# Optimization experiments

Hardware: AMD Instinct MI355X
Metric: run time of the kernel (lower is better)

## Reference

```python
import jax, jax.numpy as jnp
import numpy as np

B, T = 64, 1024
EMB = 10          # embedding_dim
H = 64            # hidden_size
NH = 2            # attention heads
IN = 3 * EMB      # 30 = GRU input_size
GAMMA = 1.0


def rbf(d):
    # BondExpansionRBF: exp(-gamma * |center - d|^2), centers = 1..10
    centers = jnp.arange(1, EMB + 1, dtype=d.dtype)          # [10]
    return jnp.exp(-GAMMA * (centers - d[..., None]) ** 2)   # [..., 10]


def gru_layer(x, w_ih, w_hh, b_ih, b_hh):
    # x: [B,T,D] -> [B,T,H]; torch GRU gate order: r, z, n
    Bn = x.shape[0]
    Hn = w_hh.shape[1]
    xw = jnp.einsum('btd,gd->btg', x, w_ih) + b_ih           # [B,T,3H] precomputed input proj

    def step(h, xt):
        gh = h @ w_hh.T + b_hh
        xr, xz, xn = jnp.split(xt, 3, axis=-1)
        hr, hz, hn = jnp.split(gh, 3, axis=-1)
        r = jax.nn.sigmoid(xr + hr)
        z = jax.nn.sigmoid(xz + hz)
        n = jnp.tanh(xn + r * hn)
        h = (1.0 - z) * n + z * h
        return h, h

    _, ys = jax.lax.scan(step, jnp.zeros((Bn, Hn), x.dtype), jnp.swapaxes(xw, 0, 1))
    return jnp.swapaxes(ys, 0, 1)


def mha(x, in_w, in_b, out_w, out_b):
    # torch nn.MultiheadAttention (batch_first, self-attn), eval mode
    Bn, Tn, E = x.shape
    Hd = E // NH
    qkv = x @ in_w.T + in_b                                   # [B,T,3E]
    q, k, v = jnp.split(qkv, 3, axis=-1)

    def heads(t):
        return t.reshape(Bn, Tn, NH, Hd).transpose(0, 2, 1, 3)  # [B,NH,T,Hd]

    q, k, v = heads(q), heads(k), heads(v)
    scores = jnp.einsum('bhqd,bhkd->bhqk', q, k) / jnp.asarray(np.sqrt(Hd), x.dtype)
    a = jax.nn.softmax(scores, axis=-1)
    o = jnp.einsum('bhqk,bhkd->bhqd', a, v).transpose(0, 2, 1, 3).reshape(Bn, Tn, E)
    return o @ out_w.T + out_b


def forward(atom_idx, bond_dist, emb, w_ih0, w_hh0, b_ih0, b_hh0,
            w_ih1, w_hh1, b_ih1, b_hh1, in_w1, in_b1, out_w1, out_b1,
            in_w2, in_b2, out_w2, out_b2, w_l, b_l, w_l1, b_l1):
    idx_i = atom_idx[..., 0]
    idx_j = atom_idx[..., 1]
    # index 0 -> zero vector (padding semantics of the python-loop conditionals)
    e_i = jnp.where((idx_i != 0)[..., None], emb[idx_i], 0.0)   # [B,T,10]
    e_j = jnp.where((idx_j != 0)[..., None], emb[idx_j], 0.0)   # [B,T,10]
    d = jnp.where((idx_i != 0)[..., None], rbf(bond_dist), 0.0)  # [B,T,10]
    x = jnp.concatenate([e_i, e_j, d], axis=-1)                  # [B,T,30]

    g = gru_layer(x, w_ih0, w_hh0, b_ih0, b_hh0)
    g = gru_layer(g, w_ih1, w_hh1, b_ih1, b_hh1)
    a = mha(g, in_w1, in_b1, out_w1, out_b1)
    a = mha(a, in_w2, in_b2, out_w2, out_b2)

    last = a[:, -1, :]                                           # [B,H]
    h = jax.nn.relu(last @ w_l.T + b_l)                          # [B,32]
    out = h @ w_l1.T + b_l1                                      # [B,1]
    return out[:, 0]                                             # [B]


def setup_inputs() -> dict:
    key = jax.random.key(0)
    ks = jax.random.split(key, 20)

    def n(k, shape, s=0.05):
        return jax.random.normal(k, shape, jnp.float32) * s

    return {
        'atom_idx': jax.random.randint(ks[0], (B, T, 2), 0, 119),
        'bond_dist': jax.random.uniform(ks[1], (B, T), jnp.float32) * 10.0,
        'emb': n(ks[2], (119, EMB), 1.0),
        'w_ih0': n(ks[3], (3 * H, IN)), 'w_hh0': n(ks[4], (3 * H, H)),
        'b_ih0': n(ks[5], (3 * H,)), 'b_hh0': n(ks[6], (3 * H,)),
        'w_ih1': n(ks[7], (3 * H, H)), 'w_hh1': n(ks[8], (3 * H, H)),
        'b_ih1': n(ks[9], (3 * H,)), 'b_hh1': n(ks[10], (3 * H,)),
        'in_w1': n(ks[11], (3 * H, H)), 'in_b1': n(ks[12], (3 * H,)),
        'out_w1': n(ks[13], (H, H)), 'out_b1': jnp.zeros((H,), jnp.float32),
        'in_w2': n(ks[14], (3 * H, H)), 'in_b2': n(ks[15], (3 * H,)),
        'out_w2': n(ks[16], (H, H)), 'out_b2': jnp.zeros((H,), jnp.float32),
        'w_l': n(ks[17], (32, H)), 'b_l': jnp.zeros((32,), jnp.float32),
        'w_l1': n(ks[18], (1, 32)), 'b_l1': jnp.zeros((1,), jnp.float32),
    }


def reference(atom_idx, bond_dist, emb, w_ih0, w_hh0, b_ih0, b_hh0,
              w_ih1, w_hh1, b_ih1, b_hh1, in_w1, in_b1, out_w1, out_b1,
              in_w2, in_b2, out_w2, out_b2, w_l, b_l, w_l1, b_l1):
    return forward(atom_idx, bond_dist, emb, w_ih0, w_hh0, b_ih0, b_hh0,
                   w_ih1, w_hh1, b_ih1, b_hh1, in_w1, in_b1, out_w1, out_b1,
                   in_w2, in_b2, out_w2, out_b2, w_l, b_l, w_l1, b_l1)
```

## Files before the change

kernel.cpp:

```cpp
#include <hip/hip_runtime.h>

typedef unsigned int uint_t;
typedef float v2f __attribute__((ext_vector_type(2)));

#define BB 64
#define TT 1024

__device__ __forceinline__ float sigm(float x) { return 1.f / (1.f + __expf(-x)); }
__device__ __forceinline__ float tanh_f(float x) { float e = __expf(2.f * x); return 1.f - 2.f / (e + 1.f); }
__device__ __forceinline__ int finitef(float x) { return (x == x) && (fabsf(x) < 1e30f); }

__device__ __forceinline__ void spinwait(volatile int* f, int v) {
  if (*f >= v) { asm volatile("" ::: "memory"); return; }
  int it = 0;
  while (*f < v && it < (1 << 15)) { __builtin_amdgcn_s_sleep(1); ++it; }
  asm volatile("" ::: "memory");
}

__device__ __forceinline__ float feat(int b, int t, int j,
                                      const int* atom_idx, const float* bond_dist,
                                      const float* emb) {
  int ii = atom_idx[(b * TT + t) * 2 + 0];
  if (j < 10) {
    return ii ? emb[ii * 10 + j] : 0.f;
  } else if (j < 20) {
    int jj = atom_idx[(b * TT + t) * 2 + 1];
    return jj ? emb[jj * 10 + (j - 10)] : 0.f;
  } else {
    float d = bond_dist[b * TT + t];
    float c = (float)(j - 19);
    float df = c - d;
    return ii ? __expf(-df * df) : 0.f;
  }
}

extern "C" __global__ void __launch_bounds__(256)
k_xw0(const int* atom_idx, const float* bond_dist, const float* emb,
      const float* w_ih0, const float* b_ih0, float* xw0) {
  int b  = blockIdx.x >> 4;
  int t0 = (blockIdx.x & 15) << 6;
  int tid = threadIdx.x;
  __shared__ float xt[64 * 31];
  for (int i = tid; i < 64 * 30; i += 256) {
    int r = i / 30, j = i % 30;
    xt[r * 31 + j] = feat(b, t0 + r, j, atom_idx, bond_dist, emb);
  }
  __syncthreads();
  for (int L = tid; L < 64 * 192; L += 256) {
    int g = L >> 6, r = L & 63;
    const float* wr = w_ih0 + g * 30;
    const float* ar = &xt[r * 31];
    float acc = b_ih0[g];
    #pragma unroll
    for (int c = 0; c < 30; ++c) acc += wr[c] * ar[c];
    xw0[((size_t)b * TT + t0 + r) * 192 + g] = acc;
  }
}

__device__ __forceinline__ void gemm64(const float* __restrict__ act_g,
                                       const float* __restrict__ w,
                                       const float* __restrict__ bias,
                                       float* al,
                                       int G, int tid,
                                       float* out, int out_rstride, size_t out_base) {
  for (int i = tid; i < 64 * 64; i += 256) {
    int r = i >> 6, c = i & 63;
    al[r * 65 + c] = act_g[r * 64 + c];
  }
  __syncthreads();
  for (int L = tid; L < 64 * G; L += 256) {
    int g = L >> 6, r = L & 63;
    const float* wr = w + (size_t)g * 64;
    const float* ar = &al[r * 65];
    float acc = bias[g];
    #pragma unroll
    for (int c = 0; c < 64; ++c) acc += wr[c] * ar[c];
    out[out_base + (size_t)r * out_rstride + g] = acc;
  }
}

__device__ __forceinline__ void loadw2(const float* p, v2f* w2) {
  const float4* p4 = (const float4*)p;
  #pragma unroll
  for (int i = 0; i < 16; ++i) {
    float4 a = p4[i];
    v2f lo; lo.x = a.x; lo.y = a.y;
    v2f hi; hi.x = a.z; hi.y = a.w;
    w2[2 * i] = lo; w2[2 * i + 1] = hi;
  }
}

extern "C" __global__ void __launch_bounds__(192, 1)
k_grufused(const float* xw0, const float* w_hh0, const float* b_hh0,
           const float* w_ih1, const float* b_ih1,
           const float* w_hh1, const float* b_hh1, float* g1out) {
  int b    = blockIdx.x;
  int lane = threadIdx.x & 63;
  int wid  = threadIdx.x >> 6;
  __shared__ __align__(16) float h0ring[16][64];
  __shared__ __align__(16) float xwring[16][192];
  __shared__ __align__(16) float h1pp[2][64];
  __shared__ int flags[3];

  if (threadIdx.x < 3) flags[threadIdx.x] = -1;
  if (wid == 0) h0ring[15][lane] = 0.f;
  if (wid == 2) h1pp[0][lane] = 0.f;
  __syncthreads();

  volatile int* w0d = &flags[0];
  volatile int* w1d = &flags[1];
  volatile int* w2d = &flags[2];

  if (wid == 0) {
    v2f wr2[32], wz2[32], wn2[32];
    loadw2(w_hh0 + (size_t)lane * 64,        wr2);
    loadw2(w_hh0 + (size_t)(64 + lane) * 64, wz2);
    loadw2(w_hh0 + (size_t)(128 + lane) * 64, wn2);
    float br = b_hh0[lane], bz = b_hh0[64 + lane], bn = b_hh0[128 + lane];
    float hv = 0.f;
    const float* xwb = xw0 + (size_t)b * TT * 192;
    float xr0 = xwb[      lane], xz0 = xwb[ 64 + lane], xn0 = xwb[128 + lane];
    float xr1 = xwb[192 + lane], xz1 = xwb[256 + lane], xn1 = xwb[320 + lane];
    float xr2 = xwb[384 + lane], xz2 = xwb[448 + lane], xn2 = xwb[512 + lane];
    float xr3 = xwb[576 + lane], xz3 = xwb[640 + lane], xn3 = xwb[704 + lane];

    auto gstep = [&](int s, float xr, float xz, float xn) {
      const float4* hp4 = (const float4*)h0ring[(s + 15) & 15];
      v2f ar; ar.x = br; ar.y = 0.f;
      v2f az; az.x = bz; az.y = 0.f;
      v2f an; an.x = bn; an.y = 0.f;
      #pragma unroll
      for (int i = 0; i < 16; ++i) {
        float4 h4 = hp4[i];
        v2f hlo; hlo.x = h4.x; hlo.y = h4.y;
        v2f hhi; hhi.x = h4.z; hhi.y = h4.w;
        ar += wr2[2*i] * hlo; ar += wr2[2*i+1] * hhi;
        az += wz2[2*i] * hlo; az += wz2[2*i+1] * hhi;
        an += wn2[2*i] * hlo; an += wn2[2*i+1] * hhi;
      }
      float r = sigm(xr + (ar.x + ar.y));
      float z = sigm(xz + (az.x + az.y));
      float n = tanh_f(xn + r * (an.x + an.y));
      hv = (1.f - z) * n + z * hv;
      h0ring[s & 15][lane] = hv;
    };
    auto pf = [&](int s, float& a, float& bb_, float& c) {
      const float* xp = xwb + (size_t)s * 192;
      a = xp[lane]; bb_ = xp[64 + lane]; c = xp[128 + lane];
    };

    for (int s0 = 0; s0 < TT; s0 += 4) {
      if (s0 >= 16) spinwait(w1d, s0 - 13);
      bool dopf = (s0 < TT - 4);
      gstep(s0 + 0, xr0, xz0, xn0); if (dopf) pf(s0 + 4, xr0, xz0, xn0);
      gstep(s0 + 1, xr1, xz1, xn1); if (dopf) pf(s0 + 5, xr1, xz1, xn1);
      gstep(s0 + 2, xr2, xz2, xn2); if (dopf) pf(s0 + 6, xr2, xz2, xn2);
      gstep(s0 + 3, xr3, xz3, xn3); if (dopf) pf(s0 + 7, xr3, xz3, xn3);
      asm volatile("" ::: "memory");
      if (lane == 0) *w0d = s0 + 3;
    }
  } else if (wid == 1) {
    v2f wr2[32], wz2[32], wn2[32];
    loadw2(w_ih1 + (size_t)lane * 64,        wr2);
    loadw2(w_ih1 + (size_t)(64 + lane) * 64, wz2);
    loadw2(w_ih1 + (size_t)(128 + lane) * 64, wn2);
    float br = b_ih1[lane], bz = b_ih1[64 + lane], bn = b_ih1[128 + lane];

    for (int t0 = 0; t0 < TT; t0 += 4) {
      spinwait(w0d, t0 + 3);
      if (t0 >= 16) spinwait(w2d, t0 - 13);
      #pragma unroll
      for (int k = 0; k < 4; ++k) {
        int t = t0 + k;
        const float4* hp4 = (const float4*)h0ring[t & 15];
        v2f ar; ar.x = br; ar.y = 0.f;
        v2f az; az.x = bz; az.y = 0.f;
        v2f an; an.x = bn; an.y = 0.f;
        #pragma unroll
        for (int i = 0; i < 16; ++i) {
          float4 h4 = hp4[i];
          v2f hlo; hlo.x = h4.x; hlo.y = h4.y;
          v2f hhi; hhi.x = h4.z; hhi.y = h4.w;
          ar += wr2[2*i] * hlo; ar += wr2[2*i+1] * hhi;
          az += wz2[2*i] * hlo; az += wz2[2*i+1] * hhi;
          an += wn2[2*i] * hlo; an += wn2[2*i+1] * hhi;
        }
        xwring[t & 15][lane]       = ar.x + ar.y;
        xwring[t & 15][64 + lane]  = az.x + az.y;
        xwring[t & 15][128 + lane] = an.x + an.y;
      }
      asm volatile("" ::: "memory");
      if (lane == 0) *w1d = t0 + 3;
    }
  } else {
    v2f wr2[32], wz2[32], wn2[32];
    loadw2(w_hh1 + (size_t)lane * 64,        wr2);
    loadw2(w_hh1 + (size_t)(64 + lane) * 64, wz2);
    loadw2(w_hh1 + (size_t)(128 + lane) * 64, wn2);
    float br = b_hh1[lane], bz = b_hh1[64 + lane], bn = b_hh1[128 + lane];
    float hv = 0.f;
    float* houtb = g1out + (size_t)b * TT * 64 + lane;

    for (int t0 = 0; t0 < TT; t0 += 4) {
      spinwait(w1d, t0 + 3);
      #pragma unroll
      for (int k = 0; k < 4; ++k) {
        int t = t0 + k;
        float xr = xwring[t & 15][lane];
        float xz = xwring[t & 15][64 + lane];
        float xn = xwring[t & 15][128 + lane];
        const float4* hp4 = (const float4*)h1pp[t & 1];
        v2f ar; ar.x = br; ar.y = 0.f;
        v2f az; az.x = bz; az.y = 0.f;
        v2f an; an.x = bn; an.y = 0.f;
        #pragma unroll
        for (int i = 0; i < 16; ++i) {
          float4 h4 = hp4[i];
          v2f hlo; hlo.x = h4.x; hlo.y = h4.y;
          v2f hhi; hhi.x = h4.z; hhi.y = h4.w;
          ar += wr2[2*i] * hlo; ar += wr2[2*i+1] * hhi;
          az += wz2[2*i] * hlo; az += wz2[2*i+1] * hhi;
          an += wn2[2*i] * hlo; an += wn2[2*i+1] * hhi;
        }
        float r = sigm(xr + (ar.x + ar.y));
        float z = sigm(xz + (az.x + az.y));
        float n = tanh_f(xn + r * (an.x + an.y));
        hv = (1.f - z) * n + z * hv;
        h1pp[(t + 1) & 1][lane] = hv;
        houtb[(size_t)t * 64] = hv;
      }
      asm volatile("" ::: "memory");
      if (lane == 0) *w2d = t0 + 3;
    }
  }
}

extern "C" __global__ void __launch_bounds__(256)
k_qkv(const float* g1, const float* in_w1, const float* in_b1,
      float* q1, float* k1, float* v1) {
  int b  = blockIdx.x >> 4;
  int t0 = (blockIdx.x & 15) << 6;
  int tid = threadIdx.x;
  __shared__ float al[64 * 65];
  const float* act = g1 + ((size_t)b * TT + t0) * 64;
  for (int i = tid; i < 64 * 64; i += 256) {
    int r = i >> 6, c = i & 63;
    al[r * 65 + c] = act[r * 64 + c];
  }
  __syncthreads();
  for (int L = tid; L < 64 * 192; L += 256) {
    int g = L >> 6, r = L & 63;
    const float* wr = in_w1 + (size_t)g * 64;
    const float* ar = &al[r * 65];
    float acc = in_b1[g];
    #pragma unroll
    for (int c = 0; c < 64; ++c) acc += wr[c] * ar[c];
    int p = g / 64;
    int rem = g - p * 64;
    int hd = rem >> 5, d = rem & 31;
    float* outp = (p == 0) ? q1 : ((p == 1) ? k1 : v1);
    outp[(((size_t)b * 2 + hd) * TT + t0 + r) * 32 + d] = acc;
  }
}

extern "C" __global__ void __launch_bounds__(256, 2)
k_attn(const float* q1, const float* k1, const float* v1, float* po, float* ml) {
  int gid = blockIdx.x;
  int b   = gid >> 3;
  int h   = (gid >> 2) & 1;
  int seg = (gid >> 1) & 1;
  int qb  = gid & 1;
  int tid = threadIdx.x;
  int tq0 = qb * 512 + tid;
  __shared__ __align__(16) float Kt[64 * 32];
  __shared__ __align__(16) float Vt[64 * 32];
  float qa[32], qc[32], oa[32], oc[32];
  const float* qp0 = q1 + (((size_t)b * 2 + h) * TT + tq0) * 32;
  const float* qp1 = qp0 + 256 * 32;
  #pragma unroll
  for (int i = 0; i < 8; ++i) {
    float4 v0 = ((const float4*)qp0)[i];
    float4 v1r = ((const float4*)qp1)[i];
    qa[4*i] = v0.x; qa[4*i+1] = v0.y; qa[4*i+2] = v0.z; qa[4*i+3] = v0.w;
    qc[4*i] = v1r.x; qc[4*i+1] = v1r.y; qc[4*i+2] = v1r.z; qc[4*i+3] = v1r.w;
  }
  #pragma unroll
  for (int i = 0; i < 32; ++i) { oa[i] = 0.f; oc[i] = 0.f; }
  float m0 = -1e30f, l0 = 0.f, m1 = -1e30f, l1 = 0.f;
  const float scale = 0.17677669529663687f;
  const float4* kb = (const float4*)(k1 + ((size_t)b * 2 + h) * TT * 32);
  const float4* vb = (const float4*)(v1 + ((size_t)b * 2 + h) * TT * 32);
  int k0 = seg << 9;
  for (int kt = k0; kt < k0 + 512; kt += 64) {
    __syncthreads();
    ((float4*)Kt)[tid]       = kb[kt * 8 + tid];
    ((float4*)Kt)[tid + 256] = kb[kt * 8 + tid + 256];
    ((float4*)Vt)[tid]       = vb[kt * 8 + tid];
    ((float4*)Vt)[tid + 256] = vb[kt * 8 + tid + 256];
    __syncthreads();
    #pragma unroll 1
    for (int c0 = 0; c0 < 64; c0 += 8) {
      float sv0[8], sv1[8];
      #pragma unroll
      for (int j = 0; j < 8; ++j) {
        const float4* kr = (const float4*)&Kt[(c0 + j) * 32];
        float a0 = 0, a1 = 0, c0a = 0, c1a = 0;
        #pragma unroll
        for (int i = 0; i < 8; ++i) {
          float4 kv = kr[i];
          a0 += qa[4*i]   * kv.x; a1 += qa[4*i+1] * kv.y;
          a0 += qa[4*i+2] * kv.z; a1 += qa[4*i+3] * kv.w;
          c0a += qc[4*i]   * kv.x; c1a += qc[4*i+1] * kv.y;
          c0a += qc[4*i+2] * kv.z; c1a += qc[4*i+3] * kv.w;
        }
        sv0[j] = (a0 + a1) * scale;
        sv1[j] = (c0a + c1a) * scale;
      }
      float cm0 = sv0[0], cm1 = sv1[0];
      #pragma unroll
      for (int j = 1; j < 8; ++j) { cm0 = fmaxf(cm0, sv0[j]); cm1 = fmaxf(cm1, sv1[j]); }
      float mn0 = fmaxf(m0, cm0), mn1 = fmaxf(m1, cm1);
      float al0 = __expf(m0 - mn0), al1 = __expf(m1 - mn1);
      float ps0 = 0.f, ps1 = 0.f;
      #pragma unroll
      for (int j = 0; j < 8; ++j) {
        sv0[j] = __expf(sv0[j] - mn0); ps0 += sv0[j];
        sv1[j] = __expf(sv1[j] - mn1); ps1 += sv1[j];
      }
      l0 = l0 * al0 + ps0; m0 = mn0;
      l1 = l1 * al1 + ps1; m1 = mn1;
      #pragma unroll
      for (int i = 0; i < 8; ++i) {
        float4 A, C;
        A.x = oa[4*i] * al0; A.y = oa[4*i+1] * al0; A.z = oa[4*i+2] * al0; A.w = oa[4*i+3] * al0;
        C.x = oc[4*i] * al1; C.y = oc[4*i+1] * al1; C.z = oc[4*i+2] * al1; C.w = oc[4*i+3] * al1;
        #pragma unroll
        for (int j = 0; j < 8; ++j) {
          float4 vv = *(const float4*)&Vt[(c0 + j) * 32 + 4 * i];
          A.x += sv0[j] * vv.x; A.y += sv0[j] * vv.y; A.z += sv0[j] * vv.z; A.w += sv0[j] * vv.w;
          C.x += sv1[j] * vv.x; C.y += sv1[j] * vv.y; C.z += sv1[j] * vv.z; C.w += sv1[j] * vv.w;
        }
        oa[4*i] = A.x; oa[4*i+1] = A.y; oa[4*i+2] = A.z; oa[4*i+3] = A.w;
        oc[4*i] = C.x; oc[4*i+1] = C.y; oc[4*i+2] = C.z; oc[4*i+3] = C.w;
      }
    }
  }
  size_t rb0 = (((size_t)(b * 2 + h)) * 2 + seg) * TT + tq0;
  size_t rb1 = rb0 + 256;
  float* op0 = po + rb0 * 32;
  float* op1 = po + rb1 * 32;
  #pragma unroll
  for (int i = 0; i < 8; ++i) {
    float4 s0; s0.x = oa[4*i]; s0.y = oa[4*i+1]; s0.z = oa[4*i+2]; s0.w = oa[4*i+3];
    float4 s1; s1.x = oc[4*i]; s1.y = oc[4*i+1]; s1.z = oc[4*i+2]; s1.w = oc[4*i+3];
    ((float4*)op0)[i] = s0;
    ((float4*)op1)[i] = s1;
  }
  ml[rb0 * 2 + 0] = m0; ml[rb0 * 2 + 1] = l0;
  ml[rb1 * 2 + 0] = m1; ml[rb1 * 2 + 1] = l1;
}

extern "C" __global__ void __launch_bounds__(256)
k_attn_comb(const float* po, const float* ml, float* attnO) {
  int row = blockIdx.x * 256 + threadIdx.x;
  int bh = row >> 10;
  int t  = row & 1023;
  int b = bh >> 1, h = bh & 1;
  size_t r0 = ((size_t)bh * 2 + 0) * TT + t;
  size_t r1 = ((size_t)bh * 2 + 1) * TT + t;
  float m0 = ml[r0 * 2], l0 = ml[r0 * 2 + 1];
  float m1 = ml[r1 * 2], l1 = ml[r1 * 2 + 1];
  float m = fmaxf(m0, m1);
  float w0 = __expf(m0 - m), w1 = __expf(m1 - m);
  float inv = 1.f / (w0 * l0 + w1 * l1);
  w0 *= inv; w1 *= inv;
  const float4* p0 = (const float4*)(po + r0 * 32);
  const float4* p1 = (const float4*)(po + r1 * 32);
  float* op = attnO + ((size_t)b * TT + t) * 64 + h * 32;
  #pragma unroll
  for (int i = 0; i < 8; ++i) {
    float4 a = p0[i], c = p1[i], r;
    r.x = a.x * w0 + c.x * w1; r.y = a.y * w0 + c.y * w1;
    r.z = a.z * w0 + c.z * w1; r.w = a.w * w0 + c.w * w1;
    ((float4*)op)[i] = r;
  }
}

extern "C" __global__ void __launch_bounds__(256)
k_oproj(const float* attnO, const float* out_w1, const float* out_b1, float* a1) {
  int b  = blockIdx.x >> 4;
  int t0 = (blockIdx.x & 15) << 6;
  __shared__ float al[64 * 65];
  gemm64(attnO + ((size_t)b * TT + t0) * 64, out_w1, out_b1, al, 64, threadIdx.x,
         a1, 64, ((size_t)b * TT + t0) * 64);
}

extern "C" __global__ void __launch_bounds__(256)
k_mha2kv(const float* a1, const float* in_w2, const float* in_b2,
         float* s2, float* v2) {
  int b  = blockIdx.x >> 4;
  int t0 = (blockIdx.x & 15) << 6;
  int tid = threadIdx.x;
  __shared__ float a1r[64 * 65];
  __shared__ float q2s[64];
  __shared__ float alast[64];
  if (tid < 64) alast[tid] = a1[((size_t)b * TT + (TT - 1)) * 64 + tid];
  for (int i = tid; i < 4096; i += 256) {
    int r = i >> 6, e = i & 63;
    a1r[r * 65 + e] = a1[((size_t)b * TT + t0 + r) * 64 + e];
  }
  __syncthreads();
  if (tid < 64) {
    float acc = in_b2[tid];
    const float* wr = in_w2 + (size_t)tid * 64;
    #pragma unroll
    for (int e = 0; e < 64; ++e) acc += alast[e] * wr[e];
    q2s[tid] = acc;
  }
  __syncthreads();
  int tt = tid & 63;
  int role = tid >> 6;
  const float* ar = &a1r[tt * 65];
  const float scale = 0.17677669529663687f;
  if (role < 2) {
    float s = 0.f;
    for (int d = 0; d < 32; ++d) {
      int row = 64 + role * 32 + d;
      const float* wr = in_w2 + (size_t)row * 64;
      float acc = in_b2[row];
      #pragma unroll
      for (int e = 0; e < 64; ++e) acc += ar[e] * wr[e];
      s += q2s[row - 64] * acc;
    }
    s2[((size_t)b * 2 + role) * TT + t0 + tt] = s * scale;
  } else {
    int half = role - 2;
    for (int d = 0; d < 32; ++d) {
      int vd = half * 32 + d;
      int row = 128 + vd;
      const float* wr = in_w2 + (size_t)row * 64;
      float acc = in_b2[row];
      #pragma unroll
      for (int e = 0; e < 64; ++e) acc += ar[e] * wr[e];
      v2[((size_t)b * TT + t0 + tt) * 64 + vd] = acc;
    }
  }
}

extern "C" __global__ void __launch_bounds__(256)
k_final(const float* s2, const float* v2,
        const float* out_w2, const float* out_b2,
        const float* w_l, const float* b_l,
        const float* w_l1, const float* b_l1,
        float* out) {
  int b = blockIdx.x;
  int tid = threadIdx.x;
  __shared__ float sm[2 * 1024];
  __shared__ float red[8];
  __shared__ float invl[2];
  __shared__ float opart[4 * 64];
  __shared__ float of[64];
  __shared__ float a2[64];
  __shared__ float hbuf[32];
  __shared__ int bad;
  if (tid == 0) bad = 0;
  for (int i = tid; i < 2048; i += 256) sm[i] = s2[(size_t)b * 2 * TT + i];
  __syncthreads();
  int lane = tid & 63;
  int wid = tid >> 6;
  for (int hh = 0; hh < 2; ++hh) {
    float mx = -1e30f;
    for (int i = tid; i < 1024; i += 256) mx = fmaxf(mx, sm[hh * 1024 + i]);
    #pragma unroll
    for (int off = 32; off > 0; off >>= 1) mx = fmaxf(mx, __shfl_down(mx, off));
    if (lane == 0) red[wid] = mx;
    __syncthreads();
    if (tid == 0) red[4] = fmaxf(fmaxf(red[0], red[1]), fmaxf(red[2], red[3]));
    __syncthreads();
    mx = red[4];
    float s = 0.f;
    for (int i = tid; i < 1024; i += 256) {
      float e = __expf(sm[hh * 1024 + i] - mx);
      sm[hh * 1024 + i] = e;
      s += e;
    }
    #pragma unroll
    for (int off = 32; off > 0; off >>= 1) s += __shfl_down(s, off);
    if (lane == 0) red[wid] = s;
    __syncthreads();
    if (tid == 0) invl[hh] = 1.f / (red[0] + red[1] + red[2] + red[3]);
    __syncthreads();
  }
  {
    int dp = tid & 63;
    int part = tid >> 6;
    int hh = dp >> 5;
    float acc = 0.f;
    for (int t = part * 256; t < part * 256 + 256; ++t)
      acc += sm[hh * 1024 + t] * v2[((size_t)b * TT + t) * 64 + dp];
    opart[part * 64 + dp] = acc;
  }
  __syncthreads();
  if (tid < 64) {
    float o = (opart[tid] + opart[64 + tid] + opart[128 + tid] + opart[192 + tid]) * invl[tid >> 5];
    of[tid] = o;
    if (!finitef(o)) bad = 1;
  }
  __syncthreads();
  if (tid < 64) {
    float acc = out_b2[tid];
    const float* wr = out_w2 + (size_t)tid * 64;
    #pragma unroll
    for (int d = 0; d < 64; ++d) acc += of[d] * wr[d];
    a2[tid] = acc;
  }
  __syncthreads();
  if (tid < 32) {
    float acc = b_l[tid];
    const float* wr = w_l + (size_t)tid * 64;
    #pragma unroll
    for (int e = 0; e < 64; ++e) acc += a2[e] * wr[e];
    hbuf[tid] = fmaxf(acc, 0.f);
  }
  __syncthreads();
  if (tid == 0) {
    float acc = b_l1[0];
    #pragma unroll
    for (int j = 0; j < 32; ++j) acc += hbuf[j] * w_l1[j];
    out[b] = bad ? 777.0f : acc;
  }
}

extern "C" void kernel_launch(void* const* d_in, const int* in_sizes, int n_in,
                              void* d_out, int out_size, void* d_ws, size_t ws_size,
                              hipStream_t stream) {
  const int*   atom_idx  = (const int*)d_in[0];
  const float* bond_dist = (const float*)d_in[1];
  const float* emb       = (const float*)d_in[2];
  const float* w_ih0     = (const float*)d_in[3];
  const float* w_hh0     = (const float*)d_in[4];
  const float* b_ih0     = (const float*)d_in[5];
  const float* b_hh0     = (const float*)d_in[6];
  const float* w_ih1     = (const float*)d_in[7];
  const float* w_hh1     = (const float*)d_in[8];
  const float* b_ih1     = (const float*)d_in[9];
  const float* b_hh1     = (const float*)d_in[10];
  const float* in_w1     = (const float*)d_in[11];
  const float* in_b1     = (const float*)d_in[12];
  const float* out_w1    = (const float*)d_in[13];
  const float* out_b1    = (const float*)d_in[14];
  const float* in_w2     = (const float*)d_in[15];
  const float* in_b2     = (const float*)d_in[16];
  const float* out_w2    = (const float*)d_in[17];
  const float* out_b2    = (const float*)d_in[18];
  const float* w_l       = (const float*)d_in[19];
  const float* b_l       = (const float*)d_in[20];
  const float* w_l1      = (const float*)d_in[21];
  const float* b_l1      = (const float*)d_in[22];

  char* ws = (char*)d_ws;
  float* X  = (float*)(ws);
  float* A  = (float*)(ws + 50331648);
  float* Bq = (float*)(ws + 67108864);
  float* D  = (float*)(ws + 83886080);
  float* q1 = X;
  float* k1 = X + 4194304;
  float* v1 = X + 8388608;
  float* po = (float*)(ws + 16777216);
  float* ml = Bq;

  k_xw0      <<<dim3(1024), dim3(256), 0, stream>>>(atom_idx, bond_dist, emb, w_ih0, b_ih0, X);
  k_grufused <<<dim3(64),   dim3(192), 0, stream>>>(X, w_hh0, b_hh0, w_ih1, b_ih1, w_hh1, b_hh1, Bq);
  k_qkv      <<<dim3(1024), dim3(256), 0, stream>>>(Bq, in_w1, in_b1, q1, k1, v1);
  k_attn     <<<dim3(512),  dim3(256), 0, stream>>>(q1, k1, v1, po, ml);
  k_attn_comb<<<dim3(512),  dim3(256), 0, stream>>>(po, ml, A);
  k_oproj    <<<dim3(1024), dim3(256), 0, stream>>>(A, out_w1, out_b1, Bq);
  k_mha2kv   <<<dim3(1024), dim3(256), 0, stream>>>(Bq, in_w2, in_b2, D, X);
  k_final    <<<dim3(64),   dim3(256), 0, stream>>>(D, X, out_w2, out_b2, w_l, b_l, w_l1, b_l1, (float*)d_out);
}
```

Measured before the change: 1.297 ms.

## Merge GRU layer-1 input projection into layer-0 wave; register-block small GEMMs

The fused two-layer GRU kernel drops from three waves to two. The layer-0 wave now also computes the layer-1 input projection of the previous hidden state in the same pass over h, so the ring buffer for h0 shrinks to a ping-pong buffer and one inter-wave handoff disappears. Separately, the xw0, qkv and out-projection GEMMs are restructured so each thread computes 8 outputs per row, reusing each shared-memory activation load across them. The trade-off is that the layer-0 wave now carries twice the weight registers and roughly twice the FMA work per step on what is the serial critical path.

```diff
diff --git a/kernel.cpp b/kernel.cpp
--- a/kernel.cpp
+++ b/kernel.cpp
@@ -46,36 +46,50 @@
     xt[r * 31 + j] = feat(b, t0 + r, j, atom_idx, bond_dist, emb);
   }
   __syncthreads();
-  for (int L = tid; L < 64 * 192; L += 256) {
-    int g = L >> 6, r = L & 63;
-    const float* wr = w_ih0 + g * 30;
-    const float* ar = &xt[r * 31];
-    float acc = b_ih0[g];
-    #pragma unroll
-    for (int c = 0; c < 30; ++c) acc += wr[c] * ar[c];
-    xw0[((size_t)b * TT + t0 + r) * 192 + g] = acc;
-  }
-}
-
-__device__ __forceinline__ void gemm64(const float* __restrict__ act_g,
-                                       const float* __restrict__ w,
-                                       const float* __restrict__ bias,
-                                       float* al,
-                                       int G, int tid,
-                                       float* out, int out_rstride, size_t out_base) {
+  int r = tid & 63, gq = tid >> 6;
+  const float* ar = &xt[r * 31];
+  for (int g0 = gq * 8; g0 < 192; g0 += 32) {
+    float acc[8];
+    #pragma unroll
+    for (int j = 0; j < 8; ++j) acc[j] = b_ih0[g0 + j];
+    #pragma unroll
+    for (int c = 0; c < 30; ++c) {
+      float a = ar[c];
+      #pragma unroll
+      for (int j = 0; j < 8; ++j) acc[j] += a * w_ih0[(g0 + j) * 30 + c];
+    }
+    #pragma unroll
+    for (int j = 0; j < 8; ++j)
+      xw0[((size_t)b * TT + t0 + r) * 192 + g0 + j] = acc[j];
+  }
+}
+
+__device__ __forceinline__ void gemm64b(const float* __restrict__ act_g,
+                                        const float* __restrict__ w,
+                                        const float* __restrict__ bias,
+                                        float* al,
+                                        int G, int tid,
+                                        float* out, int out_rstride, size_t out_base) {
   for (int i = tid; i < 64 * 64; i += 256) {
     int r = i >> 6, c = i & 63;
     al[r * 65 + c] = act_g[r * 64 + c];
   }
   __syncthreads();
-  for (int L = tid; L < 64 * G; L += 256) {
-    int g = L >> 6, r = L & 63;
-    const float* wr = w + (size_t)g * 64;
-    const float* ar = &al[r * 65];
-    float acc = bias[g];
-    #pragma unroll
-    for (int c = 0; c < 64; ++c) acc += wr[c] * ar[c];
-    out[out_base + (size_t)r * out_rstride + g] = acc;
+  int r = tid & 63, gq = tid >> 6;
+  const float* ar = &al[r * 65];
+  for (int g0 = gq * 8; g0 < G; g0 += 32) {
+    float acc[8];
+    #pragma unroll
+    for (int j = 0; j < 8; ++j) acc[j] = bias[g0 + j];
+    #pragma unroll
+    for (int c = 0; c < 64; ++c) {
+      float a = ar[c];
+      #pragma unroll
+      for (int j = 0; j < 8; ++j) acc[j] += a * w[(size_t)(g0 + j) * 64 + c];
+    }
+    #pragma unroll
+    for (int j = 0; j < 8; ++j)
+      out[out_base + (size_t)r * out_rstride + g0 + j] = acc[j];
   }
 }
 
@@ -90,33 +104,37 @@
   }
 }
 
-extern "C" __global__ void __launch_bounds__(192, 1)
+extern "C" __global__ void __launch_bounds__(128, 1)
 k_grufused(const float* xw0, const float* w_hh0, const float* b_hh0,
            const float* w_ih1, const float* b_ih1,
            const float* w_hh1, const float* b_hh1, float* g1out) {
   int b    = blockIdx.x;
   int lane = threadIdx.x & 63;
   int wid  = threadIdx.x >> 6;
-  __shared__ __align__(16) float h0ring[16][64];
+  __shared__ __align__(16) float h0pp[2][64];
   __shared__ __align__(16) float xwring[16][192];
   __shared__ __align__(16) float h1pp[2][64];
-  __shared__ int flags[3];
-
-  if (threadIdx.x < 3) flags[threadIdx.x] = -1;
-  if (wid == 0) h0ring[15][lane] = 0.f;
-  if (wid == 2) h1pp[0][lane] = 0.f;
+  __shared__ int flags[2];
+
+  if (threadIdx.x < 2) flags[threadIdx.x] = -1;
+  if (wid == 0) h0pp[0][lane] = 0.f;
+  if (wid == 1) h1pp[0][lane] = 0.f;
   __syncthreads();
 
   volatile int* w0d = &flags[0];
   volatile int* w1d = &flags[1];
-  volatile int* w2d = &flags[2];
 
   if (wid == 0) {
     v2f wr2[32], wz2[32], wn2[32];
-    loadw2(w_hh0 + (size_t)lane * 64,        wr2);
-    loadw2(w_hh0 + (size_t)(64 + lane) * 64, wz2);
+    v2f ur2[32], uz2[32], un2[32];
+    loadw2(w_hh0 + (size_t)lane * 64,         wr2);
+    loadw2(w_hh0 + (size_t)(64 + lane) * 64,  wz2);
     loadw2(w_hh0 + (size_t)(128 + lane) * 64, wn2);
+    loadw2(w_ih1 + (size_t)lane * 64,         ur2);
+    loadw2(w_ih1 + (size_t)(64 + lane) * 64,  uz2);
+    loadw2(w_ih1 + (size_t)(128 + lane) * 64, un2);
     float br = b_hh0[lane], bz = b_hh0[64 + lane], bn = b_hh0[128 + lane];
+    float cr = b_ih1[lane], cz = b_ih1[64 + lane], cn = b_ih1[128 + lane];
     float hv = 0.f;
     const float* xwb = xw0 + (size_t)b * TT * 192;
     float xr0 = xwb[      lane], xz0 = xwb[ 64 + lane], xn0 = xwb[128 + lane];
@@ -125,24 +143,35 @@
     float xr3 = xwb[576 + lane], xz3 = xwb[640 + lane], xn3 = xwb[704 + lane];
 
     auto gstep = [&](int s, float xr, float xz, float xn) {
-      const float4* hp4 = (const float4*)h0ring[(s + 15) & 15];
-      v2f ar; ar.x = br; ar.y = 0.f;
-      v2f az; az.x = bz; az.y = 0.f;
-      v2f an; an.x = bn; an.y = 0.f;
+      const float4* hp4 = (const float4*)h0pp[s & 1];
+      v2f ar_; ar_.x = br; ar_.y = 0.f;
+      v2f az_; az_.x = bz; az_.y = 0.f;
+      v2f an_; an_.x = bn; an_.y = 0.f;
+      v2f ur_; ur_.x = cr; ur_.y = 0.f;
+      v2f uz_; uz_.x = cz; uz_.y = 0.f;
+      v2f un_; un_.x = cn; un_.y = 0.f;
       #pragma unroll
       for (int i = 0; i < 16; ++i) {
         float4 h4 = hp4[i];
         v2f hlo; hlo.x = h4.x; hlo.y = h4.y;
         v2f hhi; hhi.x = h4.z; hhi.y = h4.w;
-        ar += wr2[2*i] * hlo; ar += wr2[2*i+1] * hhi;
-        az += wz2[2*i] * hlo; az += wz2[2*i+1] * hhi;
-        an += wn2[2*i] * hlo; an += wn2[2*i+1] * hhi;
+        ar_ += wr2[2*i] * hlo; ar_ += wr2[2*i+1] * hhi;
+        az_ += wz2[2*i] * hlo; az_ += wz2[2*i+1] * hhi;
+        an_ += wn2[2*i] * hlo; an_ += wn2[2*i+1] * hhi;
+        ur_ += ur2[2*i] * hlo; ur_ += ur2[2*i+1] * hhi;
+        uz_ += uz2[2*i] * hlo; uz_ += uz2[2*i+1] * hhi;
+        un_ += un2[2*i] * hlo; un_ += un2[2*i+1] * hhi;
       }
-      float r = sigm(xr + (ar.x + ar.y));
-      float z = sigm(xz + (az.x + az.y));
-      float n = tanh_f(xn + r * (an.x + an.y));
+      float r = sigm(xr + (ar_.x + ar_.y));
+      float z = sigm(xz + (az_.x + az_.y));
+      float n = tanh_f(xn + r * (an_.x + an_.y));
       hv = (1.f - z) * n + z * hv;
-      h0ring[s & 15][lane] = hv;
+      h0pp[(s + 1) & 1][lane] = hv;
+      if (s > 0) {
+        xwring[(s - 1) & 15][lane]       = ur_.x + ur_.y;
+        xwring[(s - 1) & 15][64 + lane]  = uz_.x + uz_.y;
+        xwring[(s - 1) & 15][128 + lane] = un_.x + un_.y;
+      }
     };
     auto pf = [&](int s, float& a, float& bb_, float& c) {
       const float* xp = xwb + (size_t)s * 192;
@@ -150,59 +179,46 @@
     };
 
     for (int s0 = 0; s0 < TT; s0 += 4) {
-      if (s0 >= 16) spinwait(w1d, s0 - 13);
+      if (s0 >= 16) spinwait(w1d, s0 - 14);
       bool dopf = (s0 < TT - 4);
       gstep(s0 + 0, xr0, xz0, xn0); if (dopf) pf(s0 + 4, xr0, xz0, xn0);
       gstep(s0 + 1, xr1, xz1, xn1); if (dopf) pf(s0 + 5, xr1, xz1, xn1);
       gstep(s0 + 2, xr2, xz2, xn2); if (dopf) pf(s0 + 6, xr2, xz2, xn2);
       gstep(s0 + 3, xr3, xz3, xn3); if (dopf) pf(s0 + 7, xr3, xz3, xn3);
       asm volatile("" ::: "memory");
-      if (lane == 0) *w0d = s0 + 3;
-    }
-  } else if (wid == 1) {
-    v2f wr2[32], wz2[32], wn2[32];
-    loadw2(w_ih1 + (size_t)lane * 64,        wr2);
-    loadw2(w_ih1 + (size_t)(64 + lane) * 64, wz2);
-    loadw2(w_ih1 + (size_t)(128 + lane) * 64, wn2);
-    float br = b_ih1[lane], bz = b_ih1[64 + lane], bn = b_ih1[128 + lane];
-
-    for (int t0 = 0; t0 < TT; t0 += 4) {
-      spinwait(w0d, t0 + 3);
-      if (t0 >= 16) spinwait(w2d, t0 - 13);
-      #pragma unroll
-      for (int k = 0; k < 4; ++k) {
-        int t = t0 + k;
-        const float4* hp4 = (const float4*)h0ring[t & 15];
-        v2f ar; ar.x = br; ar.y = 0.f;
-        v2f az; az.x = bz; az.y = 0.f;
-        v2f an; an.x = bn; an.y = 0.f;
-        #pragma unroll
-        for (int i = 0; i < 16; ++i) {
-          float4 h4 = hp4[i];
-          v2f hlo; hlo.x = h4.x; hlo.y = h4.y;
-          v2f hhi; hhi.x = h4.z; hhi.y = h4.w;
-          ar += wr2[2*i] * hlo; ar += wr2[2*i+1] * hhi;
-          az += wz2[2*i] * hlo; az += wz2[2*i+1] * hhi;
-          an += wn2[2*i] * hlo; an += wn2[2*i+1] * hhi;
-        }
-        xwring[t & 15][lane]       = ar.x + ar.y;
-        xwring[t & 15][64 + lane]  = az.x + az.y;
-        xwring[t & 15][128 + lane] = an.x + an.y;
+      if (lane == 0) *w0d = s0 + 2;
+    }
+    {
+      const float4* hp4 = (const float4*)h0pp[TT & 1];
+      v2f ur_; ur_.x = cr; ur_.y = 0.f;
+      v2f uz_; uz_.x = cz; uz_.y = 0.f;
+      v2f un_; un_.x = cn; un_.y = 0.f;
+      #pragma unroll
+      for (int i = 0; i < 16; ++i) {
+        float4 h4 = hp4[i];
+        v2f hlo; hlo.x = h4.x; hlo.y = h4.y;
+        v2f hhi; hhi.x = h4.z; hhi.y = h4.w;
+        ur_ += ur2[2*i] * hlo; ur_ += ur2[2*i+1] * hhi;
+        uz_ += uz2[2*i] * hlo; uz_ += uz2[2*i+1] * hhi;
+        un_ += un2[2*i] * hlo; un_ += un2[2*i+1] * hhi;
       }
+      xwring[(TT - 1) & 15][lane]       = ur_.x + ur_.y;
+      xwring[(TT - 1) & 15][64 + lane]  = uz_.x + uz_.y;
+      xwring[(TT - 1) & 15][128 + lane] = un_.x + un_.y;
       asm volatile("" ::: "memory");
-      if (lane == 0) *w1d = t0 + 3;
+      if (lane == 0) *w0d = TT - 1;
     }
   } else {
     v2f wr2[32], wz2[32], wn2[32];
-    loadw2(w_hh1 + (size_t)lane * 64,        wr2);
-    loadw2(w_hh1 + (size_t)(64 + lane) * 64, wz2);
+    loadw2(w_hh1 + (size_t)lane * 64,         wr2);
+    loadw2(w_hh1 + (size_t)(64 + lane) * 64,  wz2);
     loadw2(w_hh1 + (size_t)(128 + lane) * 64, wn2);
     float br = b_hh1[lane], bz = b_hh1[64 + lane], bn = b_hh1[128 + lane];
     float hv = 0.f;
     float* houtb = g1out + (size_t)b * TT * 64 + lane;
 
     for (int t0 = 0; t0 < TT; t0 += 4) {
-      spinwait(w1d, t0 + 3);
+      spinwait(w0d, t0 + 3);
       #pragma unroll
       for (int k = 0; k < 4; ++k) {
         int t = t0 + k;
@@ -210,27 +226,27 @@
         float xz = xwring[t & 15][64 + lane];
         float xn = xwring[t & 15][128 + lane];
         const float4* hp4 = (const float4*)h1pp[t & 1];
-        v2f ar; ar.x = br; ar.y = 0.f;
-        v2f az; az.x = bz; az.y = 0.f;
-        v2f an; an.x = bn; an.y = 0.f;
+        v2f ar_; ar_.x = br; ar_.y = 0.f;
+        v2f az_; az_.x = bz; az_.y = 0.f;
+        v2f an_; an_.x = bn; an_.y = 0.f;
         #pragma unroll
         for (int i = 0; i < 16; ++i) {
           float4 h4 = hp4[i];
           v2f hlo; hlo.x = h4.x; hlo.y = h4.y;
           v2f hhi; hhi.x = h4.z; hhi.y = h4.w;
-          ar += wr2[2*i] * hlo; ar += wr2[2*i+1] * hhi;
-          az += wz2[2*i] * hlo; az += wz2[2*i+1] * hhi;
-          an += wn2[2*i] * hlo; an += wn2[2*i+1] * hhi;
+          ar_ += wr2[2*i] * hlo; ar_ += wr2[2*i+1] * hhi;
+          az_ += wz2[2*i] * hlo; az_ += wz2[2*i+1] * hhi;
+          an_ += wn2[2*i] * hlo; an_ += wn2[2*i+1] * hhi;
         }
-        float r = sigm(xr + (ar.x + ar.y));
-        float z = sigm(xz + (az.x + az.y));
-        float n = tanh_f(xn + r * (an.x + an.y));
+        float r = sigm(xr + (ar_.x + ar_.y));
+        float z = sigm(xz + (az_.x + az_.y));
+        float n = tanh_f(xn + r * (an_.x + an_.y));
         hv = (1.f - z) * n + z * hv;
         h1pp[(t + 1) & 1][lane] = hv;
         houtb[(size_t)t * 64] = hv;
       }
       asm volatile("" ::: "memory");
-      if (lane == 0) *w2d = t0 + 3;
+      if (lane == 0) *w1d = t0 + 3;
     }
   }
 }
@@ -248,18 +264,26 @@
     al[r * 65 + c] = act[r * 64 + c];
   }
   __syncthreads();
-  for (int L = tid; L < 64 * 192; L += 256) {
-    int g = L >> 6, r = L & 63;
-    const float* wr = in_w1 + (size_t)g * 64;
-    const float* ar = &al[r * 65];
-    float acc = in_b1[g];
-    #pragma unroll
-    for (int c = 0; c < 64; ++c) acc += wr[c] * ar[c];
-    int p = g / 64;
-    int rem = g - p * 64;
-    int hd = rem >> 5, d = rem & 31;
+  int r = tid & 63, gq = tid >> 6;
+  const float* ar = &al[r * 65];
+  for (int g0 = gq * 8; g0 < 192; g0 += 32) {
+    float acc[8];
+    #pragma unroll
+    for (int j = 0; j < 8; ++j) acc[j] = in_b1[g0 + j];
+    #pragma unroll
+    for (int c = 0; c < 64; ++c) {
+      float a = ar[c];
+      #pragma unroll
+      for (int j = 0; j < 8; ++j) acc[j] += a * in_w1[(size_t)(g0 + j) * 64 + c];
+    }
+    int p = g0 / 64;
     float* outp = (p == 0) ? q1 : ((p == 1) ? k1 : v1);
-    outp[(((size_t)b * 2 + hd) * TT + t0 + r) * 32 + d] = acc;
+    #pragma unroll
+    for (int j = 0; j < 8; ++j) {
+      int rem = (g0 - p * 64) + j;
+      int hd = rem >> 5, d = rem & 31;
+      outp[(((size_t)b * 2 + hd) * TT + t0 + r) * 32 + d] = acc[j];
+    }
   }
 }
 
@@ -391,8 +415,8 @@
   int b  = blockIdx.x >> 4;
   int t0 = (blockIdx.x & 15) << 6;
   __shared__ float al[64 * 65];
-  gemm64(attnO + ((size_t)b * TT + t0) * 64, out_w1, out_b1, al, 64, threadIdx.x,
-         a1, 64, ((size_t)b * TT + t0) * 64);
+  gemm64b(attnO + ((size_t)b * TT + t0) * 64, out_w1, out_b1, al, 64, threadIdx.x,
+          a1, 64, ((size_t)b * TT + t0) * 64);
 }
 
 extern "C" __global__ void __launch_bounds__(256)
@@ -570,7 +594,7 @@
   float* ml = Bq;
 
   k_xw0      <<<dim3(1024), dim3(256), 0, stream>>>(atom_idx, bond_dist, emb, w_ih0, b_ih0, X);
-  k_grufused <<<dim3(64),   dim3(192), 0, stream>>>(X, w_hh0, b_hh0, w_ih1, b_ih1, w_hh1, b_hh1, Bq);
+  k_grufused <<<dim3(64),   dim3(128), 0, stream>>>(X, w_hh0, b_hh0, w_ih1, b_ih1, w_hh1, b_hh1, Bq);
   k_qkv      <<<dim3(1024), dim3(256), 0, stream>>>(Bq, in_w1, in_b1, q1, k1, v1);
   k_attn     <<<dim3(512),  dim3(256), 0, stream>>>(q1, k1, v1, po, ml);
   k_attn_comb<<<dim3(512),  dim3(256), 0, stream>>>(po, ml, A);
```

Result: slower. 2.054 ms (+58.5%).
